# Kernel tuning notes

Measured on AMD Instinct MI355X. Metric: run time of the kernel, lower is better.

Reference implementation:

```python
import jax, jax.numpy as jnp
import numpy as np

B, NT, D, K = 8, 64, 256, 16
NHEAD, NLEV, NPTS = 8, 4, 4
DH = D // NHEAD
LRR = 3
H, W, STRIDE = 384, 512, 4
Hf, Wf = H // STRIDE, W // STRIDE
LEVELS = [(Hf, Wf), (Hf // 2, Wf // 2), (Hf // 4, Wf // 4), (Hf // 8, Wf // 8)]
STARTS = [0]
for (hl, wl) in LEVELS[:-1]:
    STARTS.append(STARTS[-1] + hl * wl)
P = Hf * Wf
DFF = 4 * D


def _ln(x, g, b):
    m = jnp.mean(x, -1, keepdims=True)
    v = jnp.mean((x - m) ** 2, -1, keepdims=True)
    return (x - m) * jax.lax.rsqrt(v + 1e-5) * g + b


def _bilinear(v, x, y, Hl, Wl):
    # v: (BH, Hl*Wl, dh); x, y: (BH, Q) pixel coords; zero padding outside
    x0 = jnp.floor(x); y0 = jnp.floor(y)
    lx = x - x0; ly = y - y0
    x0 = x0.astype(jnp.int32); y0 = y0.astype(jnp.int32)
    def corner(xi, yi, w):
        ok = (xi >= 0) & (xi < Wl) & (yi >= 0) & (yi < Hl)
        idx = jnp.clip(yi, 0, Hl - 1) * Wl + jnp.clip(xi, 0, Wl - 1)
        g = jnp.take_along_axis(v, idx[..., None], axis=1)
        return g * (w * ok)[..., None]
    return (corner(x0, y0, (1 - lx) * (1 - ly)) + corner(x0 + 1, y0, lx * (1 - ly))
            + corner(x0, y0 + 1, (1 - lx) * ly) + corner(x0 + 1, y0 + 1, lx * ly))


def _ms_deform(value, loc, attw):
    # value: (B,S,D); loc: (B,Q,NHEAD,NLEV,NPTS,2) normalized; attw: (B,Q,NHEAD,NLEV,NPTS)
    b, s, _ = value.shape
    q = loc.shape[1]
    v = value.reshape(b, s, NHEAD, DH).transpose(0, 2, 1, 3).reshape(b * NHEAD, s, DH)
    outs = []
    for l, (hl, wl) in enumerate(LEVELS):
        vl = v[:, STARTS[l]:STARTS[l] + hl * wl]
        xy = loc[:, :, :, l].transpose(0, 2, 1, 3, 4).reshape(b * NHEAD, q * NPTS, 2)
        g = _bilinear(vl, xy[..., 0] * wl - 0.5, xy[..., 1] * hl - 0.5, hl, wl)
        outs.append(g.reshape(b, NHEAD, q, NPTS, DH))
    samp = jnp.stack(outs, axis=3)  # (B,NHEAD,Q,NLEV,NPTS,DH)
    w = attw.transpose(0, 2, 1, 3, 4)
    return jnp.einsum('bhqlp,bhqlpd->bqhd', w, samp).reshape(b, q, D)


def _forward(q_t, f4, f8, f16, f32, c_t, off_W, off_b, attw_W, attw_b, vW, vb, oW, ob,
             ln1_g, ln1_b, ffn1_W, ffn1_b, ffn2_W, ffn2_b, ln2_g, ln2_b,
             fq_W, fq_b, fk_W, fk_b, fv_W, fv_b, fo_W, fo_b, fln1_g, fln1_b,
             fffn1_W, fffn1_b, fffn2_W, fffn2_b, fln2_g, fln2_b,
             fus_W, fus_b, fin_W, fin_b, cert_W, cert_b, sc_W, sc_b):
    b, nt, d = q_t.shape
    idx = jax.lax.top_k(c_t, K)[1]  # (B,NT,K) int32, flat indices over Hf*Wf grid
    xi = (idx % Wf).astype(jnp.float32) * STRIDE + STRIDE / 2.0
    yi = (idx // Wf).astype(jnp.float32) * STRIDE + STRIDE / 2.0
    p_patch = jnp.stack([xi, yi], -1)  # (B,NT,K,2) pixel (x,y)
    ref = jnp.clip(p_patch / jnp.array([W, H], jnp.float32), 0.0, 1.0).reshape(b, nt * K, 2)
    f_scales = jnp.concatenate([f4, f8, f16, f32], axis=1)
    qk = jnp.broadcast_to(q_t[:, :, None, :], (b, nt, K, d)).reshape(b, nt * K, d)
    wh = jnp.array([[wl, hl] for (hl, wl) in LEVELS], jnp.float32)  # (NLEV,2) as (W,H)
    for l in range(LRR):
        off = (qk @ off_W[l] + off_b[l]).reshape(b, nt * K, NHEAD, NLEV, NPTS, 2)
        aw = jax.nn.softmax((qk @ attw_W[l] + attw_b[l]).reshape(b, nt * K, NHEAD, NLEV * NPTS), -1)
        aw = aw.reshape(b, nt * K, NHEAD, NLEV, NPTS)
        loc = ref[:, :, None, None, None, :] + off / wh[None, None, None, :, None, :]
        val = f_scales @ vW[l] + vb[l]
        attn = _ms_deform(val, loc, aw) @ oW[l] + ob[l]
        qk = _ln(qk + attn, ln1_g[l], ln1_b[l])
        ff = jax.nn.relu(qk @ ffn1_W[l] + ffn1_b[l]) @ ffn2_W[l] + ffn2_b[l]
        qk = _ln(qk + ff, ln2_g[l], ln2_b[l])
    qk = qk.reshape(b, nt, K, d)
    qk = jnp.concatenate([qk, jnp.broadcast_to(q_t[:, :, None, :], (b, nt, K, d))], -1)
    qk = qk @ fus_W + fus_b  # (B,NT,K,D)
    u_logit = (qk @ cert_W + cert_b)[..., 0]
    s_logit = (qk @ sc_W + sc_b)[..., 0]
    qf = q_t.reshape(b * nt, 1, d)
    kvf = qk.reshape(b * nt, K, d)
    qh = (qf @ fq_W + fq_b).reshape(b * nt, 1, NHEAD, DH)
    kh = (kvf @ fk_W + fk_b).reshape(b * nt, K, NHEAD, DH)
    vh = (kvf @ fv_W + fv_b).reshape(b * nt, K, NHEAD, DH)
    scores = jnp.einsum('bqhd,bkhd->bhqk', qh, kh) * (DH ** -0.5)
    o = jnp.einsum('bhqk,bkhd->bqhd', jax.nn.softmax(scores, -1), vh).reshape(b * nt, 1, d)
    o = _ln(qf + (o @ fo_W + fo_b), fln1_g, fln1_b)
    ff = jax.nn.relu(o @ fffn1_W + fffn1_b) @ fffn2_W + fffn2_b
    o = _ln(o + ff, fln2_g, fln2_b)
    out = jnp.concatenate([o, qf], -1) @ fin_W + fin_b
    return (out.reshape(b, nt, d), p_patch, u_logit, s_logit)


def setup_inputs() -> dict:
    ks = iter(jax.random.split(jax.random.key(0), 80))
    def rn(shape, scale=1.0):
        return jax.random.normal(next(ks), shape, jnp.float32) * scale
    s_d = D ** -0.5; s_ff = DFF ** -0.5; s_2d = (2 * D) ** -0.5
    M = NHEAD * NLEV * NPTS
    inp = dict(
        q_t=rn((B, NT, D)), f4=rn((B, P, D)), f8=rn((B, P // 4, D)),
        f16=rn((B, P // 16, D)), f32=rn((B, P // 64, D)), c_t=rn((B, NT, P)),
        off_W=rn((LRR, D, 2 * M), s_d), off_b=jnp.zeros((LRR, 2 * M)),
        attw_W=rn((LRR, D, M), s_d), attw_b=jnp.zeros((LRR, M)),
        vW=rn((LRR, D, D), s_d), vb=jnp.zeros((LRR, D)),
        oW=rn((LRR, D, D), s_d), ob=jnp.zeros((LRR, D)),
        ln1_g=jnp.ones((LRR, D)), ln1_b=jnp.zeros((LRR, D)),
        ffn1_W=rn((LRR, D, DFF), s_d), ffn1_b=jnp.zeros((LRR, DFF)),
        ffn2_W=rn((LRR, DFF, D), s_ff), ffn2_b=jnp.zeros((LRR, D)),
        ln2_g=jnp.ones((LRR, D)), ln2_b=jnp.zeros((LRR, D)),
        fq_W=rn((D, D), s_d), fq_b=jnp.zeros((D,)),
        fk_W=rn((D, D), s_d), fk_b=jnp.zeros((D,)),
        fv_W=rn((D, D), s_d), fv_b=jnp.zeros((D,)),
        fo_W=rn((D, D), s_d), fo_b=jnp.zeros((D,)),
        fln1_g=jnp.ones((D,)), fln1_b=jnp.zeros((D,)),
        fffn1_W=rn((D, DFF), s_d), fffn1_b=jnp.zeros((DFF,)),
        fffn2_W=rn((DFF, D), s_ff), fffn2_b=jnp.zeros((D,)),
        fln2_g=jnp.ones((D,)), fln2_b=jnp.zeros((D,)),
        fus_W=rn((2 * D, D), s_2d), fus_b=jnp.zeros((D,)),
        fin_W=rn((2 * D, D), s_2d), fin_b=jnp.zeros((D,)),
        cert_W=rn((D, 1), s_d), cert_b=jnp.zeros((1,)),
        sc_W=rn((D, 1), s_d), sc_b=jnp.zeros((1,)),
    )
    return inp


def reference(q_t, f4, f8, f16, f32, c_t, off_W, off_b, attw_W, attw_b, vW, vb, oW, ob,
              ln1_g, ln1_b, ffn1_W, ffn1_b, ffn2_W, ffn2_b, ln2_g, ln2_b,
              fq_W, fq_b, fk_W, fk_b, fv_W, fv_b, fo_W, fo_b, fln1_g, fln1_b,
              fffn1_W, fffn1_b, fffn2_W, fffn2_b, fln2_g, fln2_b,
              fus_W, fus_b, fin_W, fin_b, cert_W, cert_b, sc_W, sc_b):
    return _forward(q_t, f4, f8, f16, f32, c_t, off_W, off_b, attw_W, attw_b, vW, vb, oW, ob,
                    ln1_g, ln1_b, ffn1_W, ffn1_b, ffn2_W, ffn2_b, ln2_g, ln2_b,
                    fq_W, fq_b, fk_W, fk_b, fv_W, fv_b, fo_W, fo_b, fln1_g, fln1_b,
                    fffn1_W, fffn1_b, fffn2_W, fffn2_b, fln2_g, fln2_b,
                    fus_W, fus_b, fin_W, fin_b, cert_W, cert_b, sc_W, sc_b)
```

## Files before the change

kernel.cpp:

```cpp
#include <hip/hip_runtime.h>
#include <math.h>

constexpr int CB = 8, CNT = 64, CD = 256, CKSEL = 16;
constexpr int CNH = 8, CNL = 4, CNP = 4, CDH = 32;
constexpr int CP = 12288, CS = 16320, CQ = 1024, CBQ = 8192, CDFF = 1024;

using short8 = __attribute__((ext_vector_type(8))) short;
using f32x4  = __attribute__((ext_vector_type(4))) float;

__device__ __forceinline__ ushort f2bf(float f) {
  unsigned u = __float_as_uint(f);
  u += 0x7fff + ((u >> 16) & 1);
  return (ushort)(u >> 16);
}
__device__ __forceinline__ float bf2f(ushort u) {
  return __uint_as_float((unsigned)u << 16);
}

__global__ __launch_bounds__(256) void topk_kernel(const float* __restrict__ c_t,
                                                   float* __restrict__ p_patch,
                                                   float* __restrict__ ref) {
  const int bt = blockIdx.x;
  const float* row = c_t + (size_t)bt * CP;
  const int tid = threadIdx.x;
  float lv[16]; int li[16];
#pragma unroll
  for (int j = 0; j < 16; ++j) { lv[j] = -INFINITY; li[j] = 0x7fffffff; }
  for (int s = tid; s < CP; s += 256) {
    float v = row[s];
    if (v > lv[15]) {
      lv[15] = v; li[15] = s;
#pragma unroll
      for (int j = 15; j > 0; --j) {
        if (lv[j] > lv[j - 1]) {
          float tv = lv[j]; lv[j] = lv[j - 1]; lv[j - 1] = tv;
          int ti = li[j]; li[j] = li[j - 1]; li[j - 1] = ti;
        }
      }
    }
  }
  __shared__ float sv[256 * 16];
  __shared__ int   si[256 * 16];
#pragma unroll
  for (int j = 0; j < 16; ++j) { sv[tid * 16 + j] = lv[j]; si[tid * 16 + j] = li[j]; }
  __syncthreads();
  for (int step = 128; step > 0; step >>= 1) {
    float ov[16]; int oi[16];
    if (tid < step) {
      int ia = 0, ib = 0;
#pragma unroll
      for (int j = 0; j < 16; ++j) {
        bool takeA;
        if (ia >= 16) takeA = false;
        else if (ib >= 16) takeA = true;
        else {
          float av = sv[tid * 16 + ia], bv = sv[(tid + step) * 16 + ib];
          int ai = si[tid * 16 + ia], bi = si[(tid + step) * 16 + ib];
          takeA = (av > bv) || (av == bv && ai < bi);
        }
        if (takeA) { ov[j] = sv[tid * 16 + ia]; oi[j] = si[tid * 16 + ia]; ++ia; }
        else       { ov[j] = sv[(tid + step) * 16 + ib]; oi[j] = si[(tid + step) * 16 + ib]; ++ib; }
      }
    }
    __syncthreads();
    if (tid < step) {
#pragma unroll
      for (int j = 0; j < 16; ++j) { sv[tid * 16 + j] = ov[j]; si[tid * 16 + j] = oi[j]; }
    }
    __syncthreads();
  }
  if (tid < 16) {
    int idx = si[tid];
    float xi = (float)(idx & 127) * 4.0f + 2.0f;
    float yi = (float)(idx >> 7) * 4.0f + 2.0f;
    size_t o = (size_t)bt * 16 + tid;
    p_patch[o * 2 + 0] = xi;
    p_patch[o * 2 + 1] = yi;
    ref[o * 2 + 0] = fminf(fmaxf(xi * (1.0f / 512.0f), 0.f), 1.f);
    ref[o * 2 + 1] = fminf(fmaxf(yi * (1.0f / 384.0f), 0.f), 1.f);
  }
}

__global__ __launch_bounds__(256) void transpose_cvt(const float* __restrict__ src,
                                                     ushort* __restrict__ dst,
                                                     int K, int N,
                                                     size_t sStride, size_t dStride) {
  src += blockIdx.z * sStride;
  dst += blockIdx.z * dStride;
  __shared__ float t[32][33];
  const int n0 = blockIdx.x * 32, k0 = blockIdx.y * 32;
  const int c = threadIdx.x & 31, r = threadIdx.x >> 5;
#pragma unroll
  for (int i = 0; i < 4; ++i)
    t[r + i * 8][c] = src[(size_t)(k0 + r + i * 8) * N + n0 + c];
  __syncthreads();
#pragma unroll
  for (int i = 0; i < 4; ++i)
    dst[(size_t)(n0 + r + i * 8) * K + k0 + c] = f2bf(t[c][r + i * 8]);
}

struct RowVal {
  const float* f4; const float* f8; const float* f16; const float* f32;
  __device__ __forceinline__ const float* row(int r) const {
    int b = r / CS, s = r - b * CS;
    if (s < 12288) return f4 + ((size_t)b * 12288 + s) * CD;
    if (s < 15360) return f8 + ((size_t)b * 3072 + (s - 12288)) * CD;
    if (s < 16128) return f16 + ((size_t)b * 768 + (s - 15360)) * CD;
    return f32 + ((size_t)b * 192 + (s - 16128)) * CD;
  }
};

__global__ __launch_bounds__(256) void cvt_fscales(RowVal rv, ushort* __restrict__ dst) {
  size_t t = (size_t)blockIdx.x * 256 + threadIdx.x;
  size_t off = t * 8;
  int r = (int)(off >> 8);
  int c0 = (int)(off & 255);
  const float* p = rv.row(r) + c0;
  float4 a = *(const float4*)p;
  float4 b = *(const float4*)(p + 4);
  uint4 o;
  o.x = (uint)f2bf(a.x) | ((uint)f2bf(a.y) << 16);
  o.y = (uint)f2bf(a.z) | ((uint)f2bf(a.w) << 16);
  o.z = (uint)f2bf(b.x) | ((uint)f2bf(b.y) << 16);
  o.w = (uint)f2bf(b.z) | ((uint)f2bf(b.w) << 16);
  *(uint4*)(dst + off) = o;
}

__device__ __forceinline__ short8 ldfrag(const ushort* p) {
  ushort4 lo = *(const ushort4*)p;
  ushort4 hi = *(const ushort4*)(p + 4);
  short8 f;
  f[0] = (short)lo.x; f[1] = (short)lo.y; f[2] = (short)lo.z; f[3] = (short)lo.w;
  f[4] = (short)hi.x; f[5] = (short)hi.y; f[6] = (short)hi.z; f[7] = (short)hi.w;
  return f;
}

template <typename AT, typename CT, bool RELU>
__global__ __launch_bounds__(256) void gemm_mfma(const AT* __restrict__ A,
                                                 const ushort* __restrict__ Bt,
                                                 const float* __restrict__ bias,
                                                 CT* __restrict__ C, int N, int K) {
  __shared__ ushort As[128][40];
  __shared__ ushort Bs[128][40];
  const int tid = threadIdx.x;
  const int lane = tid & 63;
  const int wave = tid >> 6;
  const int wm = (wave >> 1) * 64;
  const int wn = (wave & 1) * 64;
  const int row0 = blockIdx.y * 128, col0 = blockIdx.x * 128;

  const int sr = tid >> 1;
  const int sk = (tid & 1) * 16;
  const AT*     arow = A + (size_t)(row0 + sr) * K + sk;
  const ushort* brow = Bt + (size_t)(col0 + sr) * K + sk;

  const int fr = lane & 15;
  const int fk = (lane >> 4) * 8;

  f32x4 acc[4][4] = {};
  for (int k0 = 0; k0 < K; k0 += 32) {
    if constexpr (sizeof(AT) == 4) {
      float4 a0 = *(const float4*)(arow + k0);
      float4 a1 = *(const float4*)(arow + k0 + 4);
      float4 a2 = *(const float4*)(arow + k0 + 8);
      float4 a3 = *(const float4*)(arow + k0 + 12);
      ushort4 ua0 = {f2bf(a0.x), f2bf(a0.y), f2bf(a0.z), f2bf(a0.w)};
      ushort4 ua1 = {f2bf(a1.x), f2bf(a1.y), f2bf(a1.z), f2bf(a1.w)};
      ushort4 ua2 = {f2bf(a2.x), f2bf(a2.y), f2bf(a2.z), f2bf(a2.w)};
      ushort4 ua3 = {f2bf(a3.x), f2bf(a3.y), f2bf(a3.z), f2bf(a3.w)};
      *(ushort4*)&As[sr][sk + 0]  = ua0;
      *(ushort4*)&As[sr][sk + 4]  = ua1;
      *(ushort4*)&As[sr][sk + 8]  = ua2;
      *(ushort4*)&As[sr][sk + 12] = ua3;
    } else {
      ushort4 ua0 = *(const ushort4*)(arow + k0);
      ushort4 ua1 = *(const ushort4*)(arow + k0 + 4);
      ushort4 ua2 = *(const ushort4*)(arow + k0 + 8);
      ushort4 ua3 = *(const ushort4*)(arow + k0 + 12);
      *(ushort4*)&As[sr][sk + 0]  = ua0;
      *(ushort4*)&As[sr][sk + 4]  = ua1;
      *(ushort4*)&As[sr][sk + 8]  = ua2;
      *(ushort4*)&As[sr][sk + 12] = ua3;
    }
    ushort4 ub0 = *(const ushort4*)(brow + k0);
    ushort4 ub1 = *(const ushort4*)(brow + k0 + 4);
    ushort4 ub2 = *(const ushort4*)(brow + k0 + 8);
    ushort4 ub3 = *(const ushort4*)(brow + k0 + 12);
    *(ushort4*)&Bs[sr][sk + 0]  = ub0;
    *(ushort4*)&Bs[sr][sk + 4]  = ub1;
    *(ushort4*)&Bs[sr][sk + 8]  = ub2;
    *(ushort4*)&Bs[sr][sk + 12] = ub3;
    __syncthreads();

    short8 af[4], bfr[4];
#pragma unroll
    for (int i = 0; i < 4; ++i) {
      af[i]  = ldfrag(&As[wm + i * 16 + fr][fk]);
      bfr[i] = ldfrag(&Bs[wn + i * 16 + fr][fk]);
    }
#pragma unroll
    for (int i = 0; i < 4; ++i)
#pragma unroll
      for (int j = 0; j < 4; ++j)
        acc[i][j] = __builtin_amdgcn_mfma_f32_16x16x32_bf16(af[i], bfr[j], acc[i][j], 0, 0, 0);
    __syncthreads();
  }
  const int orow = row0 + wm + (lane >> 4) * 4;
  const int ocol = col0 + wn + fr;
#pragma unroll
  for (int i = 0; i < 4; ++i)
#pragma unroll
    for (int j = 0; j < 4; ++j) {
      const int cc = ocol + j * 16;
      const float bv = bias[cc];
#pragma unroll
      for (int r = 0; r < 4; ++r) {
        float v = acc[i][j][r] + bv;
        if (RELU) v = fmaxf(v, 0.f);
        if constexpr (sizeof(CT) == 2)
          C[(size_t)(orow + i * 16 + r) * N + cc] = f2bf(v);
        else
          C[(size_t)(orow + i * 16 + r) * N + cc] = v;
      }
    }
}

__global__ void bcast_rows(const float4* __restrict__ src, float4* __restrict__ dst,
                           int n4, int shift) {
  int i = blockIdx.x * 256 + threadIdx.x;
  if (i >= n4) return;
  int r = i >> 6, j = i & 63;
  dst[i] = src[((size_t)(r >> shift) << 6) + j];
}

__global__ void concat_rows(const float4* __restrict__ s1, const float4* __restrict__ s2,
                            float4* __restrict__ dst, int n4, int shift) {
  int i = blockIdx.x * 256 + threadIdx.x;
  if (i >= n4) return;
  int r = i >> 7, j = i & 127;
  dst[i] = (j < 64) ? s1[((size_t)r << 6) + j]
                    : s2[((size_t)(r >> shift) << 6) + (j - 64)];
}

__global__ void softmax16_kernel(float* __restrict__ aw, int n) {
  int g = blockIdx.x * 256 + threadIdx.x;
  if (g >= n) return;
  float* p = aw + (size_t)g * 16;
  float mx = -INFINITY;
  for (int j = 0; j < 16; ++j) mx = fmaxf(mx, p[j]);
  float s = 0.f;
  for (int j = 0; j < 16; ++j) { float e = expf(p[j] - mx); p[j] = e; s += e; }
  float inv = 1.f / s;
  for (int j = 0; j < 16; ++j) p[j] *= inv;
}

__global__ __launch_bounds__(256) void msdeform_kernel(const ushort* __restrict__ val,
                                                       const float* __restrict__ off,
                                                       const float* __restrict__ aw,
                                                       const float* __restrict__ ref,
                                                       float* __restrict__ attn_pre) {
  const int r = blockIdx.x;
  const int b = r >> 10;
  const int tid = threadIdx.x;
  const int h = tid >> 5, c = tid & 31;
  const float rx = ref[(size_t)r * 2], ry = ref[(size_t)r * 2 + 1];
  const float* offr = off + (size_t)r * 256;
  const float* awr = aw + (size_t)r * 128;
  const ushort* vb = val + (size_t)b * CS * CD;
  float acc = 0.f;
  const int HL[4] = {96, 48, 24, 12}, WL[4] = {128, 64, 32, 16};
  const int ST[4] = {0, 12288, 15360, 16128};
#pragma unroll
  for (int l = 0; l < 4; ++l) {
    const int Hl = HL[l], Wl = WL[l], st = ST[l];
#pragma unroll
    for (int p = 0; p < 4; ++p) {
      int oi = ((h * 4 + l) * 4 + p) * 2;
      float x = rx * (float)Wl + offr[oi] - 0.5f;
      float y = ry * (float)Hl + offr[oi + 1] - 0.5f;
      float w = awr[h * 16 + l * 4 + p];
      float x0f = floorf(x), y0f = floorf(y);
      float lx = x - x0f, ly = y - y0f;
      int x0 = (int)x0f, y0 = (int)y0f;
#pragma unroll
      for (int cy = 0; cy < 2; ++cy)
#pragma unroll
        for (int cx = 0; cx < 2; ++cx) {
          int xi = x0 + cx, yi = y0 + cy;
          if (xi >= 0 && xi < Wl && yi >= 0 && yi < Hl) {
            float wc = (cx ? lx : 1.f - lx) * (cy ? ly : 1.f - ly);
            int rowi = st + yi * Wl + xi;
            acc += w * wc * bf2f(vb[(size_t)rowi * CD + h * 32 + c]);
          }
        }
    }
  }
  attn_pre[(size_t)r * 256 + tid] = acc;
}

__global__ __launch_bounds__(256) void resln_kernel(const float* __restrict__ x,
                                                    const float* __restrict__ res,
                                                    const float* __restrict__ g,
                                                    const float* __restrict__ bta,
                                                    float* __restrict__ out) {
  const int r = blockIdx.x, tid = threadIdx.x;
  const size_t off = (size_t)r * 256 + tid;
  float v = x[off] + res[off];
  __shared__ float s1[256], s2[256];
  s1[tid] = v; s2[tid] = v * v;
  __syncthreads();
  for (int st = 128; st > 0; st >>= 1) {
    if (tid < st) { s1[tid] += s1[tid + st]; s2[tid] += s2[tid + st]; }
    __syncthreads();
  }
  float m = s1[0] * (1.f / 256.f);
  float var = s2[0] * (1.f / 256.f) - m * m;
  out[off] = (v - m) * rsqrtf(var + 1e-5f) * g[tid] + bta[tid];
}

__global__ __launch_bounds__(256) void logits_kernel(const float* __restrict__ fused,
                                                     const float* __restrict__ cW, const float* __restrict__ cb,
                                                     const float* __restrict__ sW, const float* __restrict__ sb,
                                                     float* __restrict__ u, float* __restrict__ s) {
  int r = blockIdx.x * 4 + (threadIdx.x >> 6);
  int lane = threadIdx.x & 63;
  const float* row = fused + (size_t)r * 256;
  float su = 0.f, ss = 0.f;
#pragma unroll
  for (int j = 0; j < 4; ++j) {
    float v = row[lane + j * 64];
    su += v * cW[lane + j * 64];
    ss += v * sW[lane + j * 64];
  }
  for (int o = 32; o > 0; o >>= 1) { su += __shfl_down(su, o); ss += __shfl_down(ss, o); }
  if (lane == 0) { u[r] = su + cb[0]; s[r] = ss + sb[0]; }
}

__global__ __launch_bounds__(256) void attn_kernel(const float* __restrict__ qh,
                                                   const float* __restrict__ kh,
                                                   const float* __restrict__ vh,
                                                   float* __restrict__ o) {
  const int gq = blockIdx.x;
  const int tid = threadIdx.x;
  const int h = tid >> 5, d = tid & 31;
  const float q = qh[(size_t)gq * 256 + h * 32 + d];
  float sc[16];
  float mx = -INFINITY;
#pragma unroll
  for (int k = 0; k < 16; ++k) {
    float s = q * kh[((size_t)gq * 16 + k) * 256 + h * 32 + d];
#pragma unroll
    for (int o2 = 16; o2 > 0; o2 >>= 1) s += __shfl_xor(s, o2);
    s *= 0.17677669529663687f;
    sc[k] = s; mx = fmaxf(mx, s);
  }
  float den = 0.f;
#pragma unroll
  for (int k = 0; k < 16; ++k) { sc[k] = expf(sc[k] - mx); den += sc[k]; }
  float inv = 1.f / den, acc = 0.f;
#pragma unroll
  for (int k = 0; k < 16; ++k)
    acc += sc[k] * vh[((size_t)gq * 16 + k) * 256 + h * 32 + d];
  o[(size_t)gq * 256 + tid] = acc * inv;
}

constexpr size_t HALF_VAL = (size_t)CB * CS * CD / 2;
constexpr size_t OFF_FSB  = 0;
constexpr size_t OFF_VALB = OFF_FSB + HALF_VAL;
constexpr size_t OFF_QK   = OFF_VALB + HALF_VAL;
constexpr size_t OFF_TMP  = OFF_QK + (size_t)CBQ * CD;
constexpr size_t OFF_AW   = OFF_TMP + (size_t)CBQ * CD;
constexpr size_t OFF_ATT  = OFF_AW + (size_t)CBQ * 128;
constexpr size_t OFF_HID  = OFF_ATT + (size_t)CBQ * CD;
constexpr size_t OFF_REF  = OFF_HID + (size_t)CBQ * CDFF;
constexpr size_t OFF_KH   = OFF_REF + (size_t)CBQ * 2;
constexpr size_t OFF_VH   = OFF_KH + (size_t)CBQ * CD;
constexpr size_t OFF_QH   = OFF_VH + (size_t)CBQ * CD;
constexpr size_t OFF_OB   = OFF_QH + 512 * 256;
constexpr size_t OFF_T3   = OFF_OB + 512 * 256;
constexpr size_t OFF_O1   = OFF_T3 + 512 * 256;
constexpr size_t OFF_O2   = OFF_O1 + 512 * 256;
constexpr size_t OFF_FH   = OFF_O2 + 512 * 256;
constexpr size_t OFF_WT   = OFF_FH + 512 * 1024;

constexpr size_t WT_vW    = 0;
constexpr size_t WT_off   = 196608;
constexpr size_t WT_attw  = 393216;
constexpr size_t WT_oW    = 491520;
constexpr size_t WT_ffn1  = 688128;
constexpr size_t WT_ffn2  = 1474560;
constexpr size_t WT_fus   = 2260992;
constexpr size_t WT_fq    = 2392064;
constexpr size_t WT_fk    = 2457600;
constexpr size_t WT_fv    = 2523136;
constexpr size_t WT_fo    = 2588672;
constexpr size_t WT_fffn1 = 2654208;
constexpr size_t WT_fffn2 = 2916352;
constexpr size_t WT_fin   = 3178496;
constexpr size_t WT_TOTAL = 3309568;
constexpr size_t WS_NEED  = OFF_WT + (WT_TOTAL + 1) / 2;

extern "C" void kernel_launch(void* const* d_in, const int* in_sizes, int n_in,
                              void* d_out, int out_size, void* d_ws, size_t ws_size,
                              hipStream_t stream) {
  if (ws_size < WS_NEED * sizeof(float)) return;

  const float* q_t    = (const float*)d_in[0];
  const float* f4     = (const float*)d_in[1];
  const float* f8     = (const float*)d_in[2];
  const float* f16    = (const float*)d_in[3];
  const float* f32p   = (const float*)d_in[4];
  const float* c_t    = (const float*)d_in[5];
  const float* off_W  = (const float*)d_in[6];
  const float* off_b  = (const float*)d_in[7];
  const float* attw_W = (const float*)d_in[8];
  const float* attw_b = (const float*)d_in[9];
  const float* vW     = (const float*)d_in[10];
  const float* vb     = (const float*)d_in[11];
  const float* oW     = (const float*)d_in[12];
  const float* ob     = (const float*)d_in[13];
  const float* ln1_g  = (const float*)d_in[14];
  const float* ln1_b  = (const float*)d_in[15];
  const float* ffn1_W = (const float*)d_in[16];
  const float* ffn1_b = (const float*)d_in[17];
  const float* ffn2_W = (const float*)d_in[18];
  const float* ffn2_b = (const float*)d_in[19];
  const float* ln2_g  = (const float*)d_in[20];
  const float* ln2_b  = (const float*)d_in[21];
  const float* fq_W   = (const float*)d_in[22];
  const float* fq_b   = (const float*)d_in[23];
  const float* fk_W   = (const float*)d_in[24];
  const float* fk_b   = (const float*)d_in[25];
  const float* fv_W   = (const float*)d_in[26];
  const float* fv_b   = (const float*)d_in[27];
  const float* fo_W   = (const float*)d_in[28];
  const float* fo_b   = (const float*)d_in[29];
  const float* fln1_g = (const float*)d_in[30];
  const float* fln1_b = (const float*)d_in[31];
  const float* fffn1_W= (const float*)d_in[32];
  const float* fffn1_b= (const float*)d_in[33];
  const float* fffn2_W= (const float*)d_in[34];
  const float* fffn2_b= (const float*)d_in[35];
  const float* fln2_g = (const float*)d_in[36];
  const float* fln2_b = (const float*)d_in[37];
  const float* fus_W  = (const float*)d_in[38];
  const float* fus_b  = (const float*)d_in[39];
  const float* fin_W  = (const float*)d_in[40];
  const float* fin_b  = (const float*)d_in[41];
  const float* cert_W = (const float*)d_in[42];
  const float* cert_b = (const float*)d_in[43];
  const float* sc_W   = (const float*)d_in[44];
  const float* sc_b   = (const float*)d_in[45];

  float* ws = (float*)d_ws;
  float* out = (float*)d_out;

  ushort* fsb  = (ushort*)(ws + OFF_FSB);
  ushort* valb = (ushort*)(ws + OFF_VALB);
  float* qk    = ws + OFF_QK;
  float* tmp   = ws + OFF_TMP;
  float* awb   = ws + OFF_AW;
  float* attp  = ws + OFF_ATT;
  ushort* hidb = (ushort*)(ws + OFF_HID);
  float* catb  = ws + OFF_HID;
  float* ref   = ws + OFF_REF;
  float* kh    = ws + OFF_KH;
  float* vh    = ws + OFF_VH;
  float* qh    = ws + OFF_QH;
  float* obuf  = ws + OFF_OB;
  float* t3    = ws + OFF_T3;
  float* o1    = ws + OFF_O1;
  float* o2    = ws + OFF_O2;
  ushort* fhidb= (ushort*)(ws + OFF_FH);
  ushort* wt   = (ushort*)(ws + OFF_WT);

  float* out_main = out;
  float* out_pp   = out + 131072;
  float* out_u    = out + 147456;
  float* out_s    = out + 155648;

  {
    auto T = [&](const float* src, size_t wtOff, int K_, int N_, int cnt, size_t sStr, size_t dStr) {
      transpose_cvt<<<dim3(N_ / 32, K_ / 32, cnt), 256, 0, stream>>>(src, wt + wtOff, K_, N_, sStr, dStr);
    };
    T(vW,      WT_vW,    256, 256,  3, 65536, 65536);
    T(off_W,   WT_off,   256, 256,  3, 65536, 65536);
    T(attw_W,  WT_attw,  256, 128,  3, 32768, 32768);
    T(oW,      WT_oW,    256, 256,  3, 65536, 65536);
    T(ffn1_W,  WT_ffn1,  256, 1024, 3, 262144, 262144);
    T(ffn2_W,  WT_ffn2,  1024, 256, 3, 262144, 262144);
    T(fus_W,   WT_fus,   512, 256,  1, 0, 0);
    T(fq_W,    WT_fq,    256, 256,  1, 0, 0);
    T(fk_W,    WT_fk,    256, 256,  1, 0, 0);
    T(fv_W,    WT_fv,    256, 256,  1, 0, 0);
    T(fo_W,    WT_fo,    256, 256,  1, 0, 0);
    T(fffn1_W, WT_fffn1, 256, 1024, 1, 0, 0);
    T(fffn2_W, WT_fffn2, 1024, 256, 1, 0, 0);
    T(fin_W,   WT_fin,   512, 256,  1, 0, 0);
  }
  cvt_fscales<<<CB * CS * CD / 8 / 256, 256, 0, stream>>>(RowVal{f4, f8, f16, f32p}, fsb);

  topk_kernel<<<CB * CNT, 256, 0, stream>>>(c_t, out_pp, ref);

  {
    int n4 = CBQ * 64;
    bcast_rows<<<(n4 + 255) / 256, 256, 0, stream>>>((const float4*)q_t, (float4*)qk, n4, 4);
  }

  for (int l = 0; l < 3; ++l) {
    gemm_mfma<ushort, ushort, false><<<dim3(2, 1020), 256, 0, stream>>>(
        fsb, wt + WT_vW + (size_t)l * 65536, vb + l * CD, valb, 256, 256);
    gemm_mfma<float, float, false><<<dim3(2, 64), 256, 0, stream>>>(
        qk, wt + WT_off + (size_t)l * 65536, off_b + l * 256, tmp, 256, 256);
    gemm_mfma<float, float, false><<<dim3(1, 64), 256, 0, stream>>>(
        qk, wt + WT_attw + (size_t)l * 32768, attw_b + l * 128, awb, 128, 256);
    softmax16_kernel<<<(CBQ * CNH + 255) / 256, 256, 0, stream>>>(awb, CBQ * CNH);
    msdeform_kernel<<<CBQ, 256, 0, stream>>>(valb, tmp, awb, ref, attp);
    gemm_mfma<float, float, false><<<dim3(2, 64), 256, 0, stream>>>(
        attp, wt + WT_oW + (size_t)l * 65536, ob + l * CD, tmp, 256, 256);
    resln_kernel<<<CBQ, 256, 0, stream>>>(tmp, qk, ln1_g + l * CD, ln1_b + l * CD, qk);
    gemm_mfma<float, ushort, true><<<dim3(8, 64), 256, 0, stream>>>(
        qk, wt + WT_ffn1 + (size_t)l * 262144, ffn1_b + l * CDFF, hidb, 1024, 256);
    gemm_mfma<ushort, float, false><<<dim3(2, 64), 256, 0, stream>>>(
        hidb, wt + WT_ffn2 + (size_t)l * 262144, ffn2_b + l * CD, tmp, 256, 1024);
    resln_kernel<<<CBQ, 256, 0, stream>>>(tmp, qk, ln2_g + l * CD, ln2_b + l * CD, qk);
  }

  {
    int n4 = CBQ * 128;
    concat_rows<<<(n4 + 255) / 256, 256, 0, stream>>>((const float4*)qk, (const float4*)q_t,
                                                      (float4*)catb, n4, 4);
  }
  gemm_mfma<float, float, false><<<dim3(2, 64), 256, 0, stream>>>(
      catb, wt + WT_fus, fus_b, attp, 256, 512);

  logits_kernel<<<CBQ / 4, 256, 0, stream>>>(attp, cert_W, cert_b, sc_W, sc_b, out_u, out_s);

  gemm_mfma<float, float, false><<<dim3(2, 4), 256, 0, stream>>>(
      q_t, wt + WT_fq, fq_b, qh, 256, 256);
  gemm_mfma<float, float, false><<<dim3(2, 64), 256, 0, stream>>>(
      attp, wt + WT_fk, fk_b, kh, 256, 256);
  gemm_mfma<float, float, false><<<dim3(2, 64), 256, 0, stream>>>(
      attp, wt + WT_fv, fv_b, vh, 256, 256);
  attn_kernel<<<512, 256, 0, stream>>>(qh, kh, vh, obuf);

  gemm_mfma<float, float, false><<<dim3(2, 4), 256, 0, stream>>>(
      obuf, wt + WT_fo, fo_b, t3, 256, 256);
  resln_kernel<<<512, 256, 0, stream>>>(t3, q_t, fln1_g, fln1_b, o1);

  gemm_mfma<float, ushort, true><<<dim3(8, 4), 256, 0, stream>>>(
      o1, wt + WT_fffn1, fffn1_b, fhidb, 1024, 256);
  gemm_mfma<ushort, float, false><<<dim3(2, 4), 256, 0, stream>>>(
      fhidb, wt + WT_fffn2, fffn2_b, t3, 256, 1024);
  resln_kernel<<<512, 256, 0, stream>>>(t3, o1, fln2_g, fln2_b, o2);

  {
    int n4 = 512 * 128;
    concat_rows<<<(n4 + 255) / 256, 256, 0, stream>>>((const float4*)o2, (const float4*)q_t,
                                                      (float4*)catb, n4, 0);
  }
  gemm_mfma<float, float, false><<<dim3(2, 4), 256, 0, stream>>>(
      catb, wt + WT_fin, fin_b, out_main, 256, 512);
}
```

Measured before the change: 1.280 ms.

## Merge offset/attn-weight and K/V GEMMs, fuse softmax into vectorized msdeform

Concatenates the offset and attention-weight projection weights (and biases) so one GEMM produces a 384-wide output per layer, and likewise merges the final K and V projections into a single 512-wide GEMM. The softmax over 16 attention weights moves into the deformable sampling kernel, which now handles 4 queries per block with each lane gathering 4 bf16 channels through one vector load. The intent is to cut kernel launches, the extra global round trip for the attention weights, and the number of scalar gather loads. The cost is that each sampling thread now recomputes the softmax redundantly across its 8 channel lanes.

```diff
diff --git a/kernel.cpp b/kernel.cpp
--- a/kernel.cpp
+++ b/kernel.cpp
@@ -97,6 +97,13 @@
 #pragma unroll
   for (int i = 0; i < 4; ++i)
     dst[(size_t)(n0 + r + i * 8) * K + k0 + c] = f2bf(t[c][r + i * 8]);
+}
+
+__global__ void concat_bias(const float* __restrict__ a, const float* __restrict__ b,
+                            float* __restrict__ dst, int na, int nb) {
+  int i = blockIdx.x * 256 + threadIdx.x;
+  if (i < na) dst[i] = a[i];
+  else if (i < na + nb) dst[i] = b[i - na];
 }
 
 struct RowVal {
@@ -242,32 +249,30 @@
                     : s2[((size_t)(r >> shift) << 6) + (j - 64)];
 }
 
-__global__ void softmax16_kernel(float* __restrict__ aw, int n) {
-  int g = blockIdx.x * 256 + threadIdx.x;
-  if (g >= n) return;
-  float* p = aw + (size_t)g * 16;
-  float mx = -INFINITY;
-  for (int j = 0; j < 16; ++j) mx = fmaxf(mx, p[j]);
-  float s = 0.f;
-  for (int j = 0; j < 16; ++j) { float e = expf(p[j] - mx); p[j] = e; s += e; }
-  float inv = 1.f / s;
-  for (int j = 0; j < 16; ++j) p[j] *= inv;
-}
-
 __global__ __launch_bounds__(256) void msdeform_kernel(const ushort* __restrict__ val,
-                                                       const float* __restrict__ off,
-                                                       const float* __restrict__ aw,
+                                                       const float* __restrict__ oab,
                                                        const float* __restrict__ ref,
                                                        float* __restrict__ attn_pre) {
-  const int r = blockIdx.x;
+  const int tid = threadIdx.x;
+  const int r = blockIdx.x * 4 + (tid >> 6);
   const int b = r >> 10;
-  const int tid = threadIdx.x;
-  const int h = tid >> 5, c = tid & 31;
+  const int lane = tid & 63;
+  const int h = lane >> 3;
+  const int c4 = (lane & 7) * 4;
   const float rx = ref[(size_t)r * 2], ry = ref[(size_t)r * 2 + 1];
-  const float* offr = off + (size_t)r * 256;
-  const float* awr = aw + (size_t)r * 128;
-  const ushort* vb = val + (size_t)b * CS * CD;
-  float acc = 0.f;
+  const float* oa = oab + (size_t)r * 384;
+  const ushort* vb = val + (size_t)b * CS * CD + h * 32 + c4;
+
+  float ex[16];
+  float mx = -INFINITY;
+#pragma unroll
+  for (int j = 0; j < 16; ++j) { ex[j] = oa[256 + h * 16 + j]; mx = fmaxf(mx, ex[j]); }
+  float den = 0.f;
+#pragma unroll
+  for (int j = 0; j < 16; ++j) { ex[j] = expf(ex[j] - mx); den += ex[j]; }
+  const float inv = 1.f / den;
+
+  float a0 = 0.f, a1 = 0.f, a2 = 0.f, a3 = 0.f;
   const int HL[4] = {96, 48, 24, 12}, WL[4] = {128, 64, 32, 16};
   const int ST[4] = {0, 12288, 15360, 16128};
 #pragma unroll
@@ -275,10 +280,10 @@
     const int Hl = HL[l], Wl = WL[l], st = ST[l];
 #pragma unroll
     for (int p = 0; p < 4; ++p) {
-      int oi = ((h * 4 + l) * 4 + p) * 2;
-      float x = rx * (float)Wl + offr[oi] - 0.5f;
-      float y = ry * (float)Hl + offr[oi + 1] - 0.5f;
-      float w = awr[h * 16 + l * 4 + p];
+      const int oi = h * 32 + l * 8 + p * 2;
+      float x = rx * (float)Wl + oa[oi] - 0.5f;
+      float y = ry * (float)Hl + oa[oi + 1] - 0.5f;
+      float w = ex[l * 4 + p] * inv;
       float x0f = floorf(x), y0f = floorf(y);
       float lx = x - x0f, ly = y - y0f;
       int x0 = (int)x0f, y0 = (int)y0f;
@@ -288,14 +293,18 @@
         for (int cx = 0; cx < 2; ++cx) {
           int xi = x0 + cx, yi = y0 + cy;
           if (xi >= 0 && xi < Wl && yi >= 0 && yi < Hl) {
-            float wc = (cx ? lx : 1.f - lx) * (cy ? ly : 1.f - ly);
-            int rowi = st + yi * Wl + xi;
-            acc += w * wc * bf2f(vb[(size_t)rowi * CD + h * 32 + c]);
+            float wc = w * (cx ? lx : 1.f - lx) * (cy ? ly : 1.f - ly);
+            ushort4 v = *(const ushort4*)(vb + (size_t)(st + yi * Wl + xi) * CD);
+            a0 += wc * bf2f(v.x);
+            a1 += wc * bf2f(v.y);
+            a2 += wc * bf2f(v.z);
+            a3 += wc * bf2f(v.w);
           }
         }
     }
   }
-  attn_pre[(size_t)r * 256 + tid] = acc;
+  float4 o = {a0, a1, a2, a3};
+  *(float4*)(attn_pre + (size_t)r * 256 + h * 32 + c4) = o;
 }
 
 __global__ __launch_bounds__(256) void resln_kernel(const float* __restrict__ x,
@@ -337,8 +346,7 @@
 }
 
 __global__ __launch_bounds__(256) void attn_kernel(const float* __restrict__ qh,
-                                                   const float* __restrict__ kh,
-                                                   const float* __restrict__ vh,
+                                                   const float* __restrict__ kvb,
                                                    float* __restrict__ o) {
   const int gq = blockIdx.x;
   const int tid = threadIdx.x;
@@ -348,7 +356,7 @@
   float mx = -INFINITY;
 #pragma unroll
   for (int k = 0; k < 16; ++k) {
-    float s = q * kh[((size_t)gq * 16 + k) * 256 + h * 32 + d];
+    float s = q * kvb[((size_t)gq * 16 + k) * 512 + h * 32 + d];
 #pragma unroll
     for (int o2 = 16; o2 > 0; o2 >>= 1) s += __shfl_xor(s, o2);
     s *= 0.17677669529663687f;
@@ -360,7 +368,7 @@
   float inv = 1.f / den, acc = 0.f;
 #pragma unroll
   for (int k = 0; k < 16; ++k)
-    acc += sc[k] * vh[((size_t)gq * 16 + k) * 256 + h * 32 + d];
+    acc += sc[k] * kvb[((size_t)gq * 16 + k) * 512 + 256 + h * 32 + d];
   o[(size_t)gq * 256 + tid] = acc * inv;
 }
 
@@ -369,30 +377,28 @@
 constexpr size_t OFF_VALB = OFF_FSB + HALF_VAL;
 constexpr size_t OFF_QK   = OFF_VALB + HALF_VAL;
 constexpr size_t OFF_TMP  = OFF_QK + (size_t)CBQ * CD;
-constexpr size_t OFF_AW   = OFF_TMP + (size_t)CBQ * CD;
-constexpr size_t OFF_ATT  = OFF_AW + (size_t)CBQ * 128;
+constexpr size_t OFF_OAB  = OFF_TMP + (size_t)CBQ * CD;
+constexpr size_t OFF_ATT  = OFF_OAB + (size_t)CBQ * 384;
 constexpr size_t OFF_HID  = OFF_ATT + (size_t)CBQ * CD;
-constexpr size_t OFF_REF  = OFF_HID + (size_t)CBQ * CDFF;
-constexpr size_t OFF_KH   = OFF_REF + (size_t)CBQ * 2;
-constexpr size_t OFF_VH   = OFF_KH + (size_t)CBQ * CD;
-constexpr size_t OFF_QH   = OFF_VH + (size_t)CBQ * CD;
+constexpr size_t OFF_REF  = OFF_HID + (size_t)CBQ * 512;
+constexpr size_t OFF_KVB  = OFF_REF + (size_t)CBQ * 2;
+constexpr size_t OFF_QH   = OFF_KVB + (size_t)CBQ * 512;
 constexpr size_t OFF_OB   = OFF_QH + 512 * 256;
 constexpr size_t OFF_T3   = OFF_OB + 512 * 256;
 constexpr size_t OFF_O1   = OFF_T3 + 512 * 256;
 constexpr size_t OFF_O2   = OFF_O1 + 512 * 256;
 constexpr size_t OFF_FH   = OFF_O2 + 512 * 256;
-constexpr size_t OFF_WT   = OFF_FH + 512 * 1024;
+constexpr size_t OFF_CB   = OFF_FH + 262144;
+constexpr size_t OFF_WT   = OFF_CB + 2048;
 
 constexpr size_t WT_vW    = 0;
-constexpr size_t WT_off   = 196608;
-constexpr size_t WT_attw  = 393216;
+constexpr size_t WT_oab   = 196608;
 constexpr size_t WT_oW    = 491520;
 constexpr size_t WT_ffn1  = 688128;
 constexpr size_t WT_ffn2  = 1474560;
 constexpr size_t WT_fus   = 2260992;
 constexpr size_t WT_fq    = 2392064;
-constexpr size_t WT_fk    = 2457600;
-constexpr size_t WT_fv    = 2523136;
+constexpr size_t WT_fkv   = 2457600;
 constexpr size_t WT_fo    = 2588672;
 constexpr size_t WT_fffn1 = 2654208;
 constexpr size_t WT_fffn2 = 2916352;
@@ -459,19 +465,19 @@
   ushort* valb = (ushort*)(ws + OFF_VALB);
   float* qk    = ws + OFF_QK;
   float* tmp   = ws + OFF_TMP;
-  float* awb   = ws + OFF_AW;
+  float* oabuf = ws + OFF_OAB;
   float* attp  = ws + OFF_ATT;
   ushort* hidb = (ushort*)(ws + OFF_HID);
   float* catb  = ws + OFF_HID;
   float* ref   = ws + OFF_REF;
-  float* kh    = ws + OFF_KH;
-  float* vh    = ws + OFF_VH;
+  float* kvb   = ws + OFF_KVB;
   float* qh    = ws + OFF_QH;
   float* obuf  = ws + OFF_OB;
   float* t3    = ws + OFF_T3;
   float* o1    = ws + OFF_O1;
   float* o2    = ws + OFF_O2;
   ushort* fhidb= (ushort*)(ws + OFF_FH);
+  float* cbias = ws + OFF_CB;
   ushort* wt   = (ushort*)(ws + OFF_WT);
 
   float* out_main = out;
@@ -484,20 +490,25 @@
       transpose_cvt<<<dim3(N_ / 32, K_ / 32, cnt), 256, 0, stream>>>(src, wt + wtOff, K_, N_, sStr, dStr);
     };
     T(vW,      WT_vW,    256, 256,  3, 65536, 65536);
-    T(off_W,   WT_off,   256, 256,  3, 65536, 65536);
-    T(attw_W,  WT_attw,  256, 128,  3, 32768, 32768);
+    T(off_W,   WT_oab,          256, 256,  3, 65536, 98304);
+    T(attw_W,  WT_oab + 65536,  256, 128,  3, 32768, 98304);
     T(oW,      WT_oW,    256, 256,  3, 65536, 65536);
     T(ffn1_W,  WT_ffn1,  256, 1024, 3, 262144, 262144);
     T(ffn2_W,  WT_ffn2,  1024, 256, 3, 262144, 262144);
     T(fus_W,   WT_fus,   512, 256,  1, 0, 0);
     T(fq_W,    WT_fq,    256, 256,  1, 0, 0);
-    T(fk_W,    WT_fk,    256, 256,  1, 0, 0);
-    T(fv_W,    WT_fv,    256, 256,  1, 0, 0);
+    T(fk_W,    WT_fkv,          256, 256,  1, 0, 0);
+    T(fv_W,    WT_fkv + 65536,  256, 256,  1, 0, 0);
     T(fo_W,    WT_fo,    256, 256,  1, 0, 0);
     T(fffn1_W, WT_fffn1, 256, 1024, 1, 0, 0);
     T(fffn2_W, WT_fffn2, 1024, 256, 1, 0, 0);
     T(fin_W,   WT_fin,   512, 256,  1, 0, 0);
   }
+  for (int l = 0; l < 3; ++l)
+    concat_bias<<<2, 256, 0, stream>>>(off_b + l * 256, attw_b + l * 128,
+                                       cbias + l * 384, 256, 128);
+  concat_bias<<<2, 256, 0, stream>>>(fk_b, fv_b, cbias + 1152, 256, 256);
+
   cvt_fscales<<<CB * CS * CD / 8 / 256, 256, 0, stream>>>(RowVal{f4, f8, f16, f32p}, fsb);
 
   topk_kernel<<<CB * CNT, 256, 0, stream>>>(c_t, out_pp, ref);
@@ -510,12 +521,9 @@
   for (int l = 0; l < 3; ++l) {
     gemm_mfma<ushort, ushort, false><<<dim3(2, 1020), 256, 0, stream>>>(
         fsb, wt + WT_vW + (size_t)l * 65536, vb + l * CD, valb, 256, 256);
-    gemm_mfma<float, float, false><<<dim3(2, 64), 256, 0, stream>>>(
-        qk, wt + WT_off + (size_t)l * 65536, off_b + l * 256, tmp, 256, 256);
-    gemm_mfma<float, float, false><<<dim3(1, 64), 256, 0, stream>>>(
-        qk, wt + WT_attw + (size_t)l * 32768, attw_b + l * 128, awb, 128, 256);
-    softmax16_kernel<<<(CBQ * CNH + 255) / 256, 256, 0, stream>>>(awb, CBQ * CNH);
-    msdeform_kernel<<<CBQ, 256, 0, stream>>>(valb, tmp, awb, ref, attp);
+    gemm_mfma<float, float, false><<<dim3(3, 64), 256, 0, stream>>>(
+        qk, wt + WT_oab + (size_t)l * 98304, cbias + l * 384, oabuf, 384, 256);
+    msdeform_kernel<<<CBQ / 4, 256, 0, stream>>>(valb, oabuf, ref, attp);
     gemm_mfma<float, float, false><<<dim3(2, 64), 256, 0, stream>>>(
         attp, wt + WT_oW + (size_t)l * 65536, ob + l * CD, tmp, 256, 256);
     resln_kernel<<<CBQ, 256, 0, stream>>>(tmp, qk, ln1_g + l * CD, ln1_b + l * CD, qk);
@@ -538,11 +546,9 @@
 
   gemm_mfma<float, float, false><<<dim3(2, 4), 256, 0, stream>>>(
       q_t, wt + WT_fq, fq_b, qh, 256, 256);
-  gemm_mfma<float, float, false><<<dim3(2, 64), 256, 0, stream>>>(
-      attp, wt + WT_fk, fk_b, kh, 256, 256);
-  gemm_mfma<float, float, false><<<dim3(2, 64), 256, 0, stream>>>(
-      attp, wt + WT_fv, fv_b, vh, 256, 256);
-  attn_kernel<<<512, 256, 0, stream>>>(qh, kh, vh, obuf);
+  gemm_mfma<float, float, false><<<dim3(4, 64), 256, 0, stream>>>(
+      attp, wt + WT_fkv, cbias + 1152, kvb, 512, 256);
+  attn_kernel<<<512, 256, 0, stream>>>(qh, kvb, obuf);
 
   gemm_mfma<float, float, false><<<dim3(2, 4), 256, 0, stream>>>(
       obuf, wt + WT_fo, fo_b, t3, 256, 256);
```

Result: faster. 1.069 ms (-16.5%).
